# Kernel optimization log

Hardware: AMD Instinct MI355X
Metric: run time of the kernel (lower is better)

The kernel has to match this reference:

```python
import jax, jax.numpy as jnp
import numpy as np

TEMPERATURE = 0.1
NEG_INF = -1e30

def _normalize(v):
    # torch.nn.functional.normalize: v / max(||v||, 1e-12)
    n = jnp.linalg.norm(v, axis=-1, keepdims=True)
    return v / jnp.maximum(n, 1e-12)

def _line_loss(xn, yn, mx, my):
    # xn, yn: [T, D] normalized; mx, my: [T] {0,1} combined selection masks
    T = xn.shape[0]
    sim = (xn @ yn.T) / TEMPERATURE                     # [T, T]
    nx = jnp.sum(mx)
    ny = jnp.sum(my)
    # stable argsort puts selected indices first, preserving original order
    r = jnp.argsort(1 - mx)
    c = jnp.argsort(1 - my)
    sim_sel = sim[r][:, c]                              # selected block is top-left [nx, ny]
    ids = jnp.arange(T)
    masked = jnp.where((ids < nx)[:, None], sim_sel, NEG_INF)
    lse = jax.nn.logsumexp(masked, axis=0)              # column logsumexp over selected rows
    per = lse - jnp.diagonal(sim_sel)                   # = -log(exp(diag)/sum_col exp)
    m = jnp.minimum(nx, ny)                             # torch.diag length of [nx, ny] matrix
    return jnp.sum(jnp.where(ids < m, per, 0.0)) / m

def setup_inputs() -> dict:
    key = jax.random.key(0)
    k1, k2, k3, k4 = jax.random.split(key, 4)
    B, T, D = 8, 4096, 64
    x = jax.random.normal(k1, (B, T, D), dtype=jnp.float32)
    y = jax.random.normal(k2, (B, T, D), dtype=jnp.float32)
    image_masks1 = jax.random.randint(k3, (B, T), 0, 2).astype(jnp.int32)
    image_masks2 = jax.random.randint(k4, (B, T), 0, 2).astype(jnp.int32)
    shift_masks1 = jnp.ones((B, T), dtype=jnp.int32)
    shift_masks2 = jnp.ones((B, T), dtype=jnp.int32)
    return {"x": x, "y": y, "image_masks1": image_masks1, "image_masks2": image_masks2,
            "shift_masks1": shift_masks1, "shift_masks2": shift_masks2}

def reference(x, y, image_masks1, image_masks2, shift_masks1, shift_masks2):
    xn = _normalize(x)
    yn = _normalize(y)
    mx = shift_masks1 * image_masks1   # combined row selection (shift then image)
    my = shift_masks2 * image_masks2   # combined col selection
    losses = jax.vmap(_line_loss)(xn, yn, mx, my)  # [B]
    return jnp.mean(losses)
```

## Files before the change

### kernel.cpp

```cpp
#include <hip/hip_runtime.h>
#include <hip/hip_bf16.h>
#include <math.h>

#define T_DIM 4096
#define D_DIM 64
#define SPLITS 8
#define ROWS_PER_SPLIT (T_DIM / SPLITS)
#define ITERS (ROWS_PER_SPLIT / 64)
#define SCALE_X 14.4269504088896340736f
#define LN2 0.69314718055994530942f

typedef short bfrag8 __attribute__((ext_vector_type(8)));
typedef float floatx4 __attribute__((ext_vector_type(4)));

__device__ __forceinline__ float bf2f(unsigned short u) {
    return __uint_as_float(((unsigned int)u) << 16);
}

__launch_bounds__(256)
__global__ void prep(const float* __restrict__ x, const float* __restrict__ y,
                     const int* __restrict__ im1, const int* __restrict__ sh1,
                     const int* __restrict__ im2, const int* __restrict__ sh2,
                     __hip_bfloat16* __restrict__ xn, __hip_bfloat16* __restrict__ yn,
                     float* __restrict__ mxf, int* __restrict__ Ridx, int* __restrict__ Cidx,
                     int* __restrict__ cnt, float* __restrict__ gsum, float* __restrict__ out,
                     int rows, int normBlocks, int B) {
    int tid = threadIdx.x;
    if ((int)blockIdx.x < normBlocks) {
        int row = blockIdx.x * 16 + (tid >> 4);
        int l = tid & 15;
        const float* src; __hip_bfloat16* dst; float scale;
        if (row < rows) { src = x; dst = xn; scale = SCALE_X; }
        else { src = y; dst = yn; scale = 1.0f; row -= rows; }
        size_t off = (size_t)row * D_DIM + l * 4;
        float4 v = *reinterpret_cast<const float4*>(src + off);
        float ss = v.x * v.x + v.y * v.y + v.z * v.z + v.w * v.w;
        #pragma unroll
        for (int o = 1; o < 16; o <<= 1) ss += __shfl_xor(ss, o);
        float inv = scale / fmaxf(sqrtf(ss), 1e-12f);
        __hip_bfloat16 h0 = __float2bfloat16(v.x * inv);
        __hip_bfloat16 h1 = __float2bfloat16(v.y * inv);
        __hip_bfloat16 h2 = __float2bfloat16(v.z * inv);
        __hip_bfloat16 h3 = __float2bfloat16(v.w * inv);
        ushort4 o4;
        o4.x = *reinterpret_cast<unsigned short*>(&h0);
        o4.y = *reinterpret_cast<unsigned short*>(&h1);
        o4.z = *reinterpret_cast<unsigned short*>(&h2);
        o4.w = *reinterpret_cast<unsigned short*>(&h3);
        *reinterpret_cast<ushort4*>((unsigned short*)dst + off) = o4;
    } else {
        int z = blockIdx.x - normBlocks;
        int which = z & 1, b = z >> 1;
        const int* im = which ? im2 : im1;
        const int* sh = which ? sh2 : sh1;
        int* idxout   = which ? Cidx : Ridx;

        __shared__ int wtot[4], woff[4];
        __shared__ int sbase;
        int w = tid >> 6, lane = tid & 63;
        if (tid == 0) sbase = 0;

        for (int chunk = 0; chunk < T_DIM; chunk += 256) {
            int t = chunk + tid;
            int mv = im[(size_t)b * T_DIM + t] * sh[(size_t)b * T_DIM + t];
            unsigned long long bal = __ballot(mv != 0);
            int pre = __popcll(bal & ((1ull << lane) - 1ull));
            if (lane == 0) wtot[w] = __popcll(bal);
            __syncthreads();
            if (tid == 0) {
                int s = sbase;
                #pragma unroll
                for (int i = 0; i < 4; i++) { woff[i] = s; s += wtot[i]; }
                sbase = s;
            }
            __syncthreads();
            if (mv) idxout[(size_t)b * T_DIM + woff[w] + pre] = t;
            if (which == 0) mxf[(size_t)b * T_DIM + t] = (mv != 0) ? 1.0f : 0.0f;
        }
        __syncthreads();
        if (tid == 0) cnt[which * B + b] = sbase;
        if (which == 0) {
            for (int i = tid; i < T_DIM; i += 256) gsum[(size_t)b * T_DIM + i] = 0.0f;
            if (z == 0 && tid == 0) out[0] = 0.0f;
        }
    }
}

__launch_bounds__(256)
__global__ void ntxent_main(const __hip_bfloat16* __restrict__ xn,
                            const __hip_bfloat16* __restrict__ yn,
                            const float* __restrict__ mxf,
                            const int* __restrict__ Cidx,
                            const int* __restrict__ cnt,
                            float* __restrict__ gsum, int B) {
    int b  = blockIdx.y;
    int ny = cnt[B + b];
    int m  = min(cnt[b], ny);
    int j0 = blockIdx.x * 64;
    if (j0 >= m) return;
    int rbase = blockIdx.z * ROWS_PER_SPLIT;

    __shared__ __hip_bfloat16 Bs[64 * 72];
    __shared__ float sum_exp[64];
    __shared__ int   Cloc[64];

    int tid  = threadIdx.x;
    int wave = tid >> 6, lane = tid & 63, quad = lane >> 4, c16 = lane & 15;

    if (tid < 64) {
        int j = j0 + tid;
        Cloc[tid]    = (j < ny) ? Cidx[(size_t)b * T_DIM + j] : 0;
        sum_exp[tid] = 0.0f;
    }
    __syncthreads();

    #pragma unroll
    for (int i = tid; i < 64 * 8; i += 256) {
        int c = i >> 3, part = i & 7;
        bfrag8 v = *reinterpret_cast<const bfrag8*>(
            yn + ((size_t)b * T_DIM + Cloc[c]) * D_DIM + part * 8);
        *reinterpret_cast<bfrag8*>(&Bs[c * 72 + part * 8]) = v;
    }
    __syncthreads();

    bfrag8 bf[4][2];
    #pragma unroll
    for (int cg = 0; cg < 4; cg++)
        #pragma unroll
        for (int kh = 0; kh < 2; kh++)
            bf[cg][kh] = *reinterpret_cast<const bfrag8*>(
                &Bs[(cg * 16 + c16) * 72 + kh * 32 + quad * 8]);

    const __hip_bfloat16* xb = xn + (size_t)b * T_DIM * D_DIM;
    const float* mb = mxf + (size_t)b * T_DIM;

    float csum[4] = {0.f, 0.f, 0.f, 0.f};

    const __hip_bfloat16* arow = xb + (size_t)(rbase + wave * 16 + c16) * D_DIM;
    bfrag8 af0 = *reinterpret_cast<const bfrag8*>(arow + quad * 8);
    bfrag8 af1 = *reinterpret_cast<const bfrag8*>(arow + 32 + quad * 8);
    float4 mv  = *reinterpret_cast<const float4*>(mb + rbase + wave * 16 + quad * 4);

    for (int it = 0; it < ITERS; it++) {
        int it1 = (it + 1) & (ITERS - 1);
        const __hip_bfloat16* narow =
            xb + (size_t)(rbase + it1 * 64 + wave * 16 + c16) * D_DIM;
        bfrag8 naf0 = *reinterpret_cast<const bfrag8*>(narow + quad * 8);
        bfrag8 naf1 = *reinterpret_cast<const bfrag8*>(narow + 32 + quad * 8);
        float4 nmv  = *reinterpret_cast<const float4*>(
            mb + rbase + it1 * 64 + wave * 16 + quad * 4);

        float mvv[4] = {mv.x, mv.y, mv.z, mv.w};
        #pragma unroll
        for (int cg = 0; cg < 4; cg++) {
            floatx4 acc = {0.f, 0.f, 0.f, 0.f};
            acc = __builtin_amdgcn_mfma_f32_16x16x32_bf16(af0, bf[cg][0], acc, 0, 0, 0);
            acc = __builtin_amdgcn_mfma_f32_16x16x32_bf16(af1, bf[cg][1], acc, 0, 0, 0);
            #pragma unroll
            for (int r = 0; r < 4; r++)
                csum[cg] += mvv[r] * exp2f(acc[r]);
        }
        af0 = naf0; af1 = naf1; mv = nmv;
    }

    #pragma unroll
    for (int cg = 0; cg < 4; cg++) {
        csum[cg] += __shfl_xor(csum[cg], 16);
        csum[cg] += __shfl_xor(csum[cg], 32);
    }
    if (lane < 16) {
        #pragma unroll
        for (int cg = 0; cg < 4; cg++)
            atomicAdd(&sum_exp[cg * 16 + c16], csum[cg]);
    }
    __syncthreads();

    if (tid < 64)
        atomicAdd(&gsum[(size_t)b * T_DIM + j0 + tid], sum_exp[tid]);
}

__launch_bounds__(256)
__global__ void per_col_loss(const __hip_bfloat16* __restrict__ xn,
                             const __hip_bfloat16* __restrict__ yn,
                             const float* __restrict__ gsum,
                             const int* __restrict__ Ridx, const int* __restrict__ Cidx,
                             const int* __restrict__ cnt,
                             float* __restrict__ out, int B) {
    int b  = blockIdx.y;
    int m  = min(cnt[b], cnt[B + b]);
    if (m <= 0) return;

    int tid = threadIdx.x, wave = tid >> 6, lane = tid & 63;
    int g = tid >> 4, l = tid & 15;

    float acc = 0.0f;
    for (int j = blockIdx.x * 16 + g; j < m; j += 16 * gridDim.x) {
        int rj = Ridx[(size_t)b * T_DIM + j];
        int cj = Cidx[(size_t)b * T_DIM + j];
        const unsigned short* xa =
            (const unsigned short*)(xn + ((size_t)b * T_DIM + rj) * D_DIM) + l * 4;
        const unsigned short* yc =
            (const unsigned short*)(yn + ((size_t)b * T_DIM + cj) * D_DIM) + l * 4;
        float d = 0.0f;
        #pragma unroll
        for (int e = 0; e < 4; e++) d += bf2f(xa[e]) * bf2f(yc[e]);
        #pragma unroll
        for (int o = 1; o < 16; o <<= 1) d += __shfl_xor(d, o);
        if (l == 0) acc += LN2 * (__log2f(gsum[(size_t)b * T_DIM + j]) - d);
    }
    #pragma unroll
    for (int o = 1; o < 64; o <<= 1) acc += __shfl_xor(acc, o);
    __shared__ float ws[4];
    if (lane == 0) ws[wave] = acc;
    __syncthreads();
    if (tid == 0)
        atomicAdd(out, (ws[0] + ws[1] + ws[2] + ws[3]) / ((float)m * (float)B));
}

extern "C" void kernel_launch(void* const* d_in, const int* in_sizes, int n_in,
                              void* d_out, int out_size, void* d_ws, size_t ws_size,
                              hipStream_t stream) {
    const float* x  = (const float*)d_in[0];
    const float* y  = (const float*)d_in[1];
    const int* im1  = (const int*)d_in[2];
    const int* im2  = (const int*)d_in[3];
    const int* sh1  = (const int*)d_in[4];
    const int* sh2  = (const int*)d_in[5];

    int B = in_sizes[2] / T_DIM;
    int rows = B * T_DIM;
    size_t nElem = (size_t)rows * D_DIM;

    __hip_bfloat16* xn = (__hip_bfloat16*)d_ws;
    __hip_bfloat16* yn = xn + nElem;
    float* mxf  = (float*)(yn + nElem);
    float* gsum = mxf + (size_t)rows;
    int*   Ridx = (int*)(gsum + rows);
    int*   Cidx = Ridx + rows;
    int*   cnt  = Cidx + rows;

    int normBlocks = 2 * rows / 16;
    prep<<<normBlocks + 2 * B, 256, 0, stream>>>(x, y, im1, sh1, im2, sh2,
                                                 xn, yn, mxf, Ridx, Cidx, cnt,
                                                 gsum, (float*)d_out, rows, normBlocks, B);

    dim3 grid(T_DIM / 64, B, SPLITS);
    ntxent_main<<<grid, 256, 0, stream>>>(xn, yn, mxf, Cidx, cnt, gsum, B);

    dim3 grid2(16, B);
    per_col_loss<<<grid2, 256, 0, stream>>>(xn, yn, gsum, Ridx, Cidx, cnt,
                                            (float*)d_out, B);
}
```

Before: 120.6 us.

## Iterate only selected rows via compacted row indices instead of masking all rows

The main kernel now gathers rows through the compacted Ridx list and loops only up to nx, strided across splits, rather than touching all T rows and multiplying by a 0/1 mask. This skips the matmul and exp work for unselected rows (about half with random masks) and drops the mask float array. The prep kernel's scan becomes a two-pass per-wave ballot plus wave prefix scan with fewer barriers, and the shared-memory reduction before the global atomics is removed. In exchange, row loads become indirect gathers, and there are more global atomics per block.

```diff
diff --git a/kernel.cpp b/kernel.cpp
--- a/kernel.cpp
+++ b/kernel.cpp
@@ -5,8 +5,6 @@
 #define T_DIM 4096
 #define D_DIM 64
 #define SPLITS 8
-#define ROWS_PER_SPLIT (T_DIM / SPLITS)
-#define ITERS (ROWS_PER_SPLIT / 64)
 #define SCALE_X 14.4269504088896340736f
 #define LN2 0.69314718055994530942f
 
@@ -22,7 +20,7 @@
                      const int* __restrict__ im1, const int* __restrict__ sh1,
                      const int* __restrict__ im2, const int* __restrict__ sh2,
                      __hip_bfloat16* __restrict__ xn, __hip_bfloat16* __restrict__ yn,
-                     float* __restrict__ mxf, int* __restrict__ Ridx, int* __restrict__ Cidx,
+                     int* __restrict__ Ridx, int* __restrict__ Cidx,
                      int* __restrict__ cnt, float* __restrict__ gsum, float* __restrict__ out,
                      int rows, int normBlocks, int B) {
     int tid = threadIdx.x;
@@ -55,33 +53,45 @@
         const int* sh = which ? sh2 : sh1;
         int* idxout   = which ? Cidx : Ridx;
 
-        __shared__ int wtot[4], woff[4];
-        __shared__ int sbase;
+        __shared__ int cw[64];
+        __shared__ int offx[64];
         int w = tid >> 6, lane = tid & 63;
-        if (tid == 0) sbase = 0;
-
-        for (int chunk = 0; chunk < T_DIM; chunk += 256) {
-            int t = chunk + tid;
-            int mv = im[(size_t)b * T_DIM + t] * sh[(size_t)b * T_DIM + t];
+        const int* imb = im + (size_t)b * T_DIM;
+        const int* shb = sh + (size_t)b * T_DIM;
+
+        #pragma unroll
+        for (int k = 0; k < 16; k++) {
+            int u = w + k * 4;
+            int t = u * 64 + lane;
+            int mv = imb[t] * shb[t];
+            unsigned long long bal = __ballot(mv != 0);
+            if (lane == 0) cw[u] = __popcll(bal);
+        }
+        __syncthreads();
+        if (w == 0) {
+            int v = cw[lane];
+            int incl = v;
+            #pragma unroll
+            for (int o = 1; o < 64; o <<= 1) {
+                int t = __shfl_up(incl, o);
+                if (lane >= o) incl += t;
+            }
+            offx[lane] = incl - v;
+            if (lane == 63) cnt[which * B + b] = incl;
+        }
+        __syncthreads();
+        #pragma unroll
+        for (int k = 0; k < 16; k++) {
+            int u = w + k * 4;
+            int t = u * 64 + lane;
+            int mv = imb[t] * shb[t];
             unsigned long long bal = __ballot(mv != 0);
             int pre = __popcll(bal & ((1ull << lane) - 1ull));
-            if (lane == 0) wtot[w] = __popcll(bal);
-            __syncthreads();
-            if (tid == 0) {
-                int s = sbase;
-                #pragma unroll
-                for (int i = 0; i < 4; i++) { woff[i] = s; s += wtot[i]; }
-                sbase = s;
-            }
-            __syncthreads();
-            if (mv) idxout[(size_t)b * T_DIM + woff[w] + pre] = t;
-            if (which == 0) mxf[(size_t)b * T_DIM + t] = (mv != 0) ? 1.0f : 0.0f;
-        }
-        __syncthreads();
-        if (tid == 0) cnt[which * B + b] = sbase;
+            if (mv) idxout[(size_t)b * T_DIM + offx[u] + pre] = t;
+        }
         if (which == 0) {
             for (int i = tid; i < T_DIM; i += 256) gsum[(size_t)b * T_DIM + i] = 0.0f;
-            if (z == 0 && tid == 0) out[0] = 0.0f;
+            if (b == 0 && tid == 0) out[0] = 0.0f;
         }
     }
 }
@@ -89,28 +99,27 @@
 __launch_bounds__(256)
 __global__ void ntxent_main(const __hip_bfloat16* __restrict__ xn,
                             const __hip_bfloat16* __restrict__ yn,
-                            const float* __restrict__ mxf,
+                            const int* __restrict__ Ridx,
                             const int* __restrict__ Cidx,
                             const int* __restrict__ cnt,
                             float* __restrict__ gsum, int B) {
     int b  = blockIdx.y;
+    int nx = cnt[b];
     int ny = cnt[B + b];
-    int m  = min(cnt[b], ny);
+    int m  = min(nx, ny);
     int j0 = blockIdx.x * 64;
     if (j0 >= m) return;
-    int rbase = blockIdx.z * ROWS_PER_SPLIT;
+    int rbase = blockIdx.z * 64;
 
     __shared__ __hip_bfloat16 Bs[64 * 72];
-    __shared__ float sum_exp[64];
-    __shared__ int   Cloc[64];
+    __shared__ int Cloc[64];
 
     int tid  = threadIdx.x;
     int wave = tid >> 6, lane = tid & 63, quad = lane >> 4, c16 = lane & 15;
 
     if (tid < 64) {
         int j = j0 + tid;
-        Cloc[tid]    = (j < ny) ? Cidx[(size_t)b * T_DIM + j] : 0;
-        sum_exp[tid] = 0.0f;
+        Cloc[tid] = (j < ny) ? Cidx[(size_t)b * T_DIM + j] : 0;
     }
     __syncthreads();
 
@@ -132,25 +141,28 @@
                 &Bs[(cg * 16 + c16) * 72 + kh * 32 + quad * 8]);
 
     const __hip_bfloat16* xb = xn + (size_t)b * T_DIM * D_DIM;
-    const float* mb = mxf + (size_t)b * T_DIM;
+    const int* Rb = Ridx + (size_t)b * T_DIM;
 
     float csum[4] = {0.f, 0.f, 0.f, 0.f};
 
-    const __hip_bfloat16* arow = xb + (size_t)(rbase + wave * 16 + c16) * D_DIM;
+    int gi = rbase + wave * 16 + c16;
+    int idx0 = (gi < nx) ? Rb[gi] : 0;
+    const __hip_bfloat16* arow = xb + (size_t)idx0 * D_DIM;
     bfrag8 af0 = *reinterpret_cast<const bfrag8*>(arow + quad * 8);
     bfrag8 af1 = *reinterpret_cast<const bfrag8*>(arow + 32 + quad * 8);
-    float4 mv  = *reinterpret_cast<const float4*>(mb + rbase + wave * 16 + quad * 4);
-
-    for (int it = 0; it < ITERS; it++) {
-        int it1 = (it + 1) & (ITERS - 1);
-        const __hip_bfloat16* narow =
-            xb + (size_t)(rbase + it1 * 64 + wave * 16 + c16) * D_DIM;
+
+    for (int i0 = rbase; i0 < nx; i0 += 64 * SPLITS) {
+        int gin = i0 + 64 * SPLITS + wave * 16 + c16;
+        int idxn = (gin < nx) ? Rb[gin] : 0;
+        const __hip_bfloat16* narow = xb + (size_t)idxn * D_DIM;
         bfrag8 naf0 = *reinterpret_cast<const bfrag8*>(narow + quad * 8);
         bfrag8 naf1 = *reinterpret_cast<const bfrag8*>(narow + 32 + quad * 8);
-        float4 nmv  = *reinterpret_cast<const float4*>(
-            mb + rbase + it1 * 64 + wave * 16 + quad * 4);
-
-        float mvv[4] = {mv.x, mv.y, mv.z, mv.w};
+
+        int grow0 = i0 + wave * 16 + quad * 4;
+        float wv[4];
+        #pragma unroll
+        for (int r = 0; r < 4; r++) wv[r] = (grow0 + r < nx) ? 1.0f : 0.0f;
+
         #pragma unroll
         for (int cg = 0; cg < 4; cg++) {
             floatx4 acc = {0.f, 0.f, 0.f, 0.f};
@@ -158,9 +170,9 @@
             acc = __builtin_amdgcn_mfma_f32_16x16x32_bf16(af1, bf[cg][1], acc, 0, 0, 0);
             #pragma unroll
             for (int r = 0; r < 4; r++)
-                csum[cg] += mvv[r] * exp2f(acc[r]);
-        }
-        af0 = naf0; af1 = naf1; mv = nmv;
+                csum[cg] += wv[r] * exp2f(acc[r]);
+        }
+        af0 = naf0; af1 = naf1;
     }
 
     #pragma unroll
@@ -171,12 +183,8 @@
     if (lane < 16) {
         #pragma unroll
         for (int cg = 0; cg < 4; cg++)
-            atomicAdd(&sum_exp[cg * 16 + c16], csum[cg]);
-    }
-    __syncthreads();
-
-    if (tid < 64)
-        atomicAdd(&gsum[(size_t)b * T_DIM + j0 + tid], sum_exp[tid]);
+            atomicAdd(&gsum[(size_t)b * T_DIM + j0 + cg * 16 + c16], csum[cg]);
+    }
 }
 
 __launch_bounds__(256)
@@ -233,19 +241,18 @@
 
     __hip_bfloat16* xn = (__hip_bfloat16*)d_ws;
     __hip_bfloat16* yn = xn + nElem;
-    float* mxf  = (float*)(yn + nElem);
-    float* gsum = mxf + (size_t)rows;
+    float* gsum = (float*)(yn + nElem);
     int*   Ridx = (int*)(gsum + rows);
     int*   Cidx = Ridx + rows;
     int*   cnt  = Cidx + rows;
 
     int normBlocks = 2 * rows / 16;
     prep<<<normBlocks + 2 * B, 256, 0, stream>>>(x, y, im1, sh1, im2, sh2,
-                                                 xn, yn, mxf, Ridx, Cidx, cnt,
+                                                 xn, yn, Ridx, Cidx, cnt,
                                                  gsum, (float*)d_out, rows, normBlocks, B);
 
     dim3 grid(T_DIM / 64, B, SPLITS);
-    ntxent_main<<<grid, 256, 0, stream>>>(xn, yn, mxf, Cidx, cnt, gsum, B);
+    ntxent_main<<<grid, 256, 0, stream>>>(xn, yn, Ridx, Cidx, cnt, gsum, B);
 
     dim3 grid2(16, B);
     per_col_loss<<<grid2, 256, 0, stream>>>(xn, yn, gsum, Ridx, Cidx, cnt,
```

Result: faster. 108.4 us (-10.1%).
